# Kernel optimization log

Measured on AMD Instinct MI355X. Metric: run time of the kernel, lower is better.

## Reference

```python
import jax, jax.numpy as jnp
import numpy as np

B, S, D = 2, 2048, 2048
NH, NKV, HD = 16, 4, 128
REP = NH // NKV
EPS = 1e-6
ROPE_THETA = 1e6


def setup_inputs() -> dict:
    key = jax.random.key(0)
    ks = jax.random.split(key, 6)
    x = jax.random.normal(ks[0], (B, S, D), jnp.float32)
    # real rotary embeddings: [S, HD]
    inv_freq = 1.0 / (ROPE_THETA ** (np.arange(0, HD, 2, dtype=np.float64) / HD))
    freqs = np.outer(np.arange(S, dtype=np.float64), inv_freq)
    emb = np.concatenate([freqs, freqs], axis=-1)
    cos = jnp.asarray(np.cos(emb), jnp.float32)
    sin = jnp.asarray(np.sin(emb), jnp.float32)
    scale = 1.0 / np.sqrt(D)
    Wq = jax.random.normal(ks[1], (D, NH * HD), jnp.float32) * scale   # [in, out]
    Wk = jax.random.normal(ks[2], (D, NKV * HD), jnp.float32) * scale
    Wv = jax.random.normal(ks[3], (D, NKV * HD), jnp.float32) * scale
    Wo = jax.random.normal(ks[4], (NH * HD, D), jnp.float32) * (1.0 / np.sqrt(NH * HD))
    q_norm_w = jnp.ones((HD,), jnp.float32)
    k_norm_w = jnp.ones((HD,), jnp.float32)
    return dict(x=x, cos=cos, sin=sin, Wq=Wq, Wk=Wk, Wv=Wv, Wo=Wo,
                q_norm_w=q_norm_w, k_norm_w=k_norm_w)


def _rms_norm(h, w):
    var = jnp.mean(h * h, axis=-1, keepdims=True)
    return w * (h * jax.lax.rsqrt(var + EPS))


def _rotate_half(h):
    h1, h2 = jnp.split(h, 2, axis=-1)
    return jnp.concatenate([-h2, h1], axis=-1)


def reference(x, cos, sin, Wq, Wk, Wv, Wo, q_norm_w, k_norm_w):
    b, s, _ = x.shape
    q = (x @ Wq).reshape(b, s, NH, HD)
    k = (x @ Wk).reshape(b, s, NKV, HD)
    v = (x @ Wv).reshape(b, s, NKV, HD)
    # per-head QK RMSNorm
    q = _rms_norm(q, q_norm_w)
    k = _rms_norm(k, k_norm_w)
    # RoPE: cos/sin [S,HD] -> broadcast over batch and heads
    c = cos[None, :, None, :]
    s_ = sin[None, :, None, :]
    q = q * c + _rotate_half(q) * s_
    k = k * c + _rotate_half(k) * s_
    # GQA: group q heads per kv head instead of materializing repeat_kv
    qg = q.reshape(b, s, NKV, REP, HD)
    scores = jnp.einsum('bqgrd,bkgd->bgrqk', qg, k) / np.sqrt(HD)
    causal = jnp.tril(jnp.ones((s, s), bool))  # [q,k]
    scores = jnp.where(causal, scores, -jnp.inf)
    probs = jax.nn.softmax(scores.astype(jnp.float32), axis=-1).astype(q.dtype)
    out = jnp.einsum('bgrqk,bkgd->bqgrd', probs, v).reshape(b, s, NH * HD)
    return out @ Wo
```

## Files before the change

### kernel.cpp

```cpp
#include <hip/hip_runtime.h>
#include <hip/hip_bf16.h>
#include <math.h>

#define B_ 2
#define S_ 2048
#define D_ 2048
#define NH_ 16
#define NKV_ 4
#define HD_ 128
#define EPS_ 1e-6f
#define SCALE_ 0.08838834764831845f
#define LOG2E_ 1.4426950408889634f
#define KOFF_ 2048
#define VOFF_ 2560

typedef float f32x4 __attribute__((ext_vector_type(4)));
typedef short bf16x8 __attribute__((ext_vector_type(8)));
typedef short short4v __attribute__((ext_vector_type(4)));
typedef float float4v __attribute__((ext_vector_type(4)));
typedef unsigned uint2v __attribute__((ext_vector_type(2)));

static __device__ __forceinline__ short f2bf(float f) {
    union { float f; unsigned u; } x{f};
    unsigned r = (x.u + 0x7fff + ((x.u >> 16) & 1)) >> 16;
    return (short)r;
}
static __device__ __forceinline__ float bf2f(short s) {
    union { unsigned u; float f; } x; x.u = ((unsigned)(unsigned short)s) << 16; return x.f;
}
static __device__ __forceinline__ unsigned pack_bf2(float a, float b) {
    return __builtin_amdgcn_perm(__builtin_bit_cast(unsigned, b),
                                 __builtin_bit_cast(unsigned, a), 0x07060302u);
}

#define AS1(p) ((const __attribute__((address_space(1))) void*)(p))
#define AS3(p) ((__attribute__((address_space(3))) void*)(p))
static __device__ __forceinline__ void async16(const void* g, void* l) {
    __builtin_amdgcn_global_load_lds(AS1(g), AS3(l), 16, 0, 0);
}

__global__ __launch_bounds__(256) void cast_kernel(const float* __restrict__ in,
                                                   short* __restrict__ out) {
    size_t i = ((size_t)blockIdx.x * 256 + threadIdx.x) * 4;
    float4v v = *(const float4v*)(in + i);
    short4v o; o.x = f2bf(v.x); o.y = f2bf(v.y); o.z = f2bf(v.z); o.w = f2bf(v.w);
    *(short4v*)(out + i) = o;
}

__global__ __launch_bounds__(256) void transpose_all_kernel(const float* __restrict__ Wq,
                                                            const float* __restrict__ Wk,
                                                            const float* __restrict__ Wv,
                                                            const float* __restrict__ Wo,
                                                            short* __restrict__ Wt,
                                                            short* __restrict__ Wot) {
    __shared__ float tile[64][65];
    const int bx = blockIdx.x, by = blockIdx.y;
    const float* src; short* dst; int N, nb;
    if (bx < 32)      { src = Wq; dst = Wt;                         N = 2048; nb = bx; }
    else if (bx < 40) { src = Wk; dst = Wt + (size_t)KOFF_ * 2048;  N = 512;  nb = bx - 32; }
    else if (bx < 48) { src = Wv; dst = Wt + (size_t)VOFF_ * 2048;  N = 512;  nb = bx - 40; }
    else              { src = Wo; dst = Wot;                        N = 2048; nb = bx - 48; }
    const int n0 = nb * 64, k0 = by * 64;
    const int tid = threadIdx.x;
    for (int r = 0; r < 16; ++r) {
        int k = r * 4 + (tid >> 6);
        int n = tid & 63;
        tile[k][n] = src[(size_t)(k0 + k) * N + n0 + n];
    }
    __syncthreads();
    for (int r = 0; r < 4; ++r) {
        int n  = r * 16 + (tid >> 4);
        int kk = (tid & 15) * 4;
        short4v o4;
        o4.x = f2bf(tile[kk + 0][n]); o4.y = f2bf(tile[kk + 1][n]);
        o4.z = f2bf(tile[kk + 2][n]); o4.w = f2bf(tile[kk + 3][n]);
        *(short4v*)&dst[(size_t)(n0 + n) * 2048 + k0 + kk] = o4;
    }
}

template<typename TC>
__global__ __launch_bounds__(256) void gemm_tt_kernel(const short* __restrict__ A,
                                                      const short* __restrict__ Bt,
                                                      TC* __restrict__ C,
                                                      int M, int N, int K) {
    __shared__ short As[128 * 32];
    __shared__ short Bs[128 * 32];

    const int tid  = threadIdx.x;
    const int bn   = blockIdx.x, bm = blockIdx.y;
    const int wave = tid >> 6, lane = tid & 63;
    const int quad = lane >> 4, l16 = lane & 15;
    const int wr = wave >> 1, wc = wave & 1;

    f32x4 acc[4][4];
    for (int i = 0; i < 4; ++i)
        for (int j = 0; j < 4; ++j) acc[i][j] = (f32x4){0.f, 0.f, 0.f, 0.f};

    const short* Abase = A  + (size_t)(bm * 128) * K;
    const short* Bbase = Bt + (size_t)(bn * 128) * K;

    int ci0 = wave * 128 + lane;
    for (int k0 = 0; k0 < K; k0 += 32) {
        __syncthreads();
        for (int t = 0; t < 2; ++t) {
            int ci = ci0 + t * 64;
            int r  = ci >> 2;
            int c  = ((ci & 3) - (r >> 1)) & 3;
            size_t goff = (size_t)r * K + k0 + c * 8;
            async16(Abase + goff, &As[ci * 8]);
            async16(Bbase + goff, &Bs[ci * 8]);
        }
        __syncthreads();

        bf16x8 af[4], bfv[4];
        for (int mt = 0; mt < 4; ++mt) {
            int r = wr * 64 + mt * 16 + l16;
            af[mt] = *(const bf16x8*)&As[r * 32 + (((quad + (r >> 1)) & 3) * 8)];
        }
        for (int nt = 0; nt < 4; ++nt) {
            int r = wc * 64 + nt * 16 + l16;
            bfv[nt] = *(const bf16x8*)&Bs[r * 32 + (((quad + (r >> 1)) & 3) * 8)];
        }
        for (int mt = 0; mt < 4; ++mt)
            for (int nt = 0; nt < 4; ++nt)
                acc[mt][nt] = __builtin_amdgcn_mfma_f32_16x16x32_bf16(
                    af[mt], bfv[nt], acc[mt][nt], 0, 0, 0);
    }

    for (int mt = 0; mt < 4; ++mt)
        for (int nt = 0; nt < 4; ++nt)
            for (int j = 0; j < 4; ++j) {
                int row = bm * 128 + wr * 64 + mt * 16 + quad * 4 + j;
                int col = bn * 128 + wc * 64 + nt * 16 + l16;
                float v = acc[mt][nt][j];
                if constexpr (__is_same(TC, short))
                    C[(size_t)row * N + col] = f2bf(v);
                else
                    C[(size_t)row * N + col] = v;
            }
}

__global__ __launch_bounds__(256) void qkv_fused_kernel(const short* __restrict__ xb,
                                                        const short* __restrict__ Wt,
                                                        const float* __restrict__ cosb,
                                                        const float* __restrict__ sinb,
                                                        const float* __restrict__ qw,
                                                        const float* __restrict__ kw,
                                                        short* __restrict__ q_rope,
                                                        short* __restrict__ k_rope,
                                                        short* __restrict__ vtr) {
    __shared__ short tile[128 * 128];
    __shared__ float ss2[2][128];
    short* As = tile;
    short* Bs = tile + 4096;

    const int tid  = threadIdx.x;
    const int bn   = blockIdx.x, bm = blockIdx.y;
    const int wave = tid >> 6, lane = tid & 63;
    const int quad = lane >> 4, l16 = lane & 15;
    const int wr = wave >> 1, wc = wave & 1;

    f32x4 acc[4][4];
    for (int i = 0; i < 4; ++i)
        for (int j = 0; j < 4; ++j) acc[i][j] = (f32x4){0.f, 0.f, 0.f, 0.f};

    const short* Abase = xb + (size_t)(bm * 128) * 2048;
    const short* Bbase = Wt + (size_t)(bn * 128) * 2048;

    int ci0 = wave * 128 + lane;
    for (int k0 = 0; k0 < 2048; k0 += 32) {
        __syncthreads();
        for (int t = 0; t < 2; ++t) {
            int ci = ci0 + t * 64;
            int r  = ci >> 2;
            int c  = ((ci & 3) - (r >> 1)) & 3;
            size_t goff = (size_t)r * 2048 + k0 + c * 8;
            async16(Abase + goff, &As[ci * 8]);
            async16(Bbase + goff, &Bs[ci * 8]);
        }
        __syncthreads();

        bf16x8 af[4], bfv[4];
        for (int mt = 0; mt < 4; ++mt) {
            int r = wr * 64 + mt * 16 + l16;
            af[mt] = *(const bf16x8*)&As[r * 32 + (((quad + (r >> 1)) & 3) * 8)];
        }
        for (int nt = 0; nt < 4; ++nt) {
            int r = wc * 64 + nt * 16 + l16;
            bfv[nt] = *(const bf16x8*)&Bs[r * 32 + (((quad + (r >> 1)) & 3) * 8)];
        }
        for (int mt = 0; mt < 4; ++mt)
            for (int nt = 0; nt < 4; ++nt)
                acc[mt][nt] = __builtin_amdgcn_mfma_f32_16x16x32_bf16(
                    af[mt], bfv[nt], acc[mt][nt], 0, 0, 0);
    }

    if (bn >= 20) {
        const int g = bn - 20;
        for (int mt = 0; mt < 4; ++mt) {
            int tok0 = bm * 128 + wr * 64 + mt * 16 + quad * 4;
            int bb = tok0 >> 11, s0 = tok0 & (S_ - 1);
            for (int nt = 0; nt < 4; ++nt) {
                int d = wc * 64 + nt * 16 + l16;
                short4v o4;
                o4.x = f2bf(acc[mt][nt][0]); o4.y = f2bf(acc[mt][nt][1]);
                o4.z = f2bf(acc[mt][nt][2]); o4.w = f2bf(acc[mt][nt][3]);
                *(short4v*)&vtr[((size_t)(bb * NKV_ + g) * HD_ + d) * S_ + s0] = o4;
            }
        }
        return;
    }

    __syncthreads();
    {
        float pss[4][4];
        for (int mt = 0; mt < 4; ++mt)
            for (int j = 0; j < 4; ++j) {
                float s = 0.f;
                for (int nt = 0; nt < 4; ++nt) s += acc[mt][nt][j] * acc[mt][nt][j];
                pss[mt][j] = s;
            }
        for (int off = 1; off < 16; off <<= 1)
            for (int mt = 0; mt < 4; ++mt)
                for (int j = 0; j < 4; ++j)
                    pss[mt][j] += __shfl_xor(pss[mt][j], off);
        if (l16 == 0)
            for (int mt = 0; mt < 4; ++mt)
                for (int j = 0; j < 4; ++j)
                    ss2[wc][wr * 64 + mt * 16 + quad * 4 + j] = pss[mt][j];
    }
    for (int mt = 0; mt < 4; ++mt)
        for (int nt = 0; nt < 4; ++nt)
            for (int j = 0; j < 4; ++j)
                tile[(wr * 64 + mt * 16 + quad * 4 + j) * 128 + wc * 64 + nt * 16 + l16]
                    = f2bf(acc[mt][nt][j]);
    __syncthreads();

    const bool isQ = (bn < 16);
    const float osc = isQ ? (SCALE_ * LOG2E_) : 1.0f;
    const float* w = isQ ? qw : kw;
    for (int it = 0; it < 8; ++it) {
        int idx = tid + it * 256;
        int row = idx >> 4, seg = idx & 15;
        int tok = bm * 128 + row;
        int bb = tok >> 11, s = tok & (S_ - 1);
        float rstd = rsqrtf((ss2[0][row] + ss2[1][row]) * (1.0f / HD_) + EPS_);
        int c0 = seg * 8, p0 = (seg ^ 8) * 8;
        bf16x8 ta = *(const bf16x8*)&tile[row * 128 + c0];
        bf16x8 tb = *(const bf16x8*)&tile[row * 128 + p0];
        float sgn = (seg < 8) ? -1.0f : 1.0f;
        unsigned ov[4];
        for (int i2 = 0; i2 < 4; ++i2) {
            float r0, r1;
            for (int k = 0; k < 2; ++k) {
                int i = i2 * 2 + k;
                float n1 = bf2f(ta[i]) * rstd * w[c0 + i];
                float n2 = bf2f(tb[i]) * rstd * w[p0 + i];
                float cs = cosb[(size_t)s * HD_ + c0 + i];
                float sn = sinb[(size_t)s * HD_ + c0 + i];
                float o = (n1 * cs + sgn * n2 * sn) * osc;
                if (k == 0) r0 = o; else r1 = o;
            }
            ov[i2] = ((unsigned)(unsigned short)f2bf(r0)) |
                     ((unsigned)(unsigned short)f2bf(r1) << 16);
        }
        short* dst = isQ
            ? q_rope + ((size_t)(bb * S_ + s) * NH_ + bn) * HD_ + c0
            : k_rope + ((size_t)(bb * NKV_ + (bn - 16)) * S_ + s) * HD_ + c0;
        uint2v w0; w0.x = ov[0]; w0.y = ov[1];
        uint2v w1; w1.x = ov[2]; w1.y = ov[3];
        *(uint2v*)dst = w0;
        *(uint2v*)(dst + 4) = w1;
    }
}

__global__ __launch_bounds__(256, 2) void attn_kernel(const short* __restrict__ qr,
                                                      const short* __restrict__ kg,
                                                      const short* __restrict__ vt,
                                                      short* __restrict__ aout) {
    __shared__ short Ks[2][64 * 128];
    __shared__ short Vs[2][128 * 64];

    const int lin = blockIdx.x;
    const int b  = lin & 1;
    const int g  = (lin >> 1) & 3;
    const int hq = (lin >> 3) & 3;
    const int pr = lin >> 5;
    const int h  = g * 4 + hq;

    const int wave = threadIdx.x >> 6, lane = threadIdx.x & 63;
    const int quad = lane >> 4, l16 = lane & 15;

    const short* kbase = kg + (size_t)(b * NKV_ + g) * S_ * HD_;
    const short* vbase = vt + (size_t)(b * NKV_ + g) * HD_ * S_;

    for (int pass = 0; pass < 2; ++pass) {
        const int qt    = pass ? (31 - pr) : pr;
        const int iters = qt + 1;
        const int qrow  = qt * 64 + wave * 16 + l16;

        bf16x8 qf[4];
        {
            const short* qp = qr + ((size_t)(b * S_ + qrow) * NH_ + h) * HD_;
            for (int ks = 0; ks < 4; ++ks)
                qf[ks] = *(const bf16x8*)(qp + ks * 32 + quad * 8);
        }

        f32x4 o[8];
        for (int i = 0; i < 8; ++i) o[i] = (f32x4){0.f, 0.f, 0.f, 0.f};
        float m_i = -INFINITY, l_i = 0.f;

        auto stage = [&](int kt, int bsel) {
            const short* kt_base = kbase + (size_t)kt * 64 * HD_;
            const short* vt_base = vbase + kt * 64;
            for (int t = 0; t < 4; ++t) {
                int ci  = (wave * 4 + t) * 64 + lane;
                int key = ci >> 4;
                int c   = (ci & 15) ^ ((key ^ (key >> 2)) & 15);
                async16(kt_base + key * HD_ + c * 8, &Ks[bsel][ci * 8]);
            }
            for (int t = 0; t < 4; ++t) {
                int ci = (wave * 4 + t) * 64 + lane;
                int d  = ci >> 3;
                int c  = (ci & 7) ^ (d & 7);
                async16(vt_base + (size_t)d * S_ + c * 8, &Vs[bsel][ci * 8]);
            }
        };

        stage(0, 0);
        int buf = 0;
        for (int kt = 0; kt < iters; ++kt) {
            __syncthreads();
            if (kt + 1 < iters) stage(kt + 1, buf ^ 1);

            f32x4 acc[4];
            for (int t = 0; t < 4; ++t) acc[t] = (f32x4){0.f, 0.f, 0.f, 0.f};
            for (int t = 0; t < 4; ++t) {
                int lk = ((t >> 1) << 5) + ((l16 >> 2) << 3) + ((t & 1) << 2) + (l16 & 3);
                const short* kp = &Ks[buf][lk * 128];
                int pm = (lk ^ (lk >> 2)) & 15;
                for (int ks = 0; ks < 4; ++ks) {
                    bf16x8 kf = *(const bf16x8*)(kp + (((ks * 4 + quad) ^ pm) * 8));
                    acc[t] = __builtin_amdgcn_mfma_f32_16x16x32_bf16(kf, qf[ks], acc[t], 0, 0, 0);
                }
            }
            const int key_base = kt * 64;
            if (key_base + 63 > qt * 64 + wave * 16) {
                for (int t = 0; t < 4; ++t)
                    for (int j = 0; j < 4; ++j) {
                        int kl = key_base + ((t >> 1) << 5) + (quad << 3) + ((t & 1) << 2) + j;
                        if (kl > qrow) acc[t][j] = -INFINITY;
                    }
            }
            float mx = m_i;
            for (int t = 0; t < 4; ++t)
                for (int j = 0; j < 4; ++j) mx = fmaxf(mx, acc[t][j]);
            mx = fmaxf(mx, __shfl_xor(mx, 16));
            mx = fmaxf(mx, __shfl_xor(mx, 32));
            float al = __builtin_amdgcn_exp2f(m_i - mx);
            m_i = mx;
            float rs = 0.f;
            float p[4][4];
            for (int t = 0; t < 4; ++t)
                for (int j = 0; j < 4; ++j) {
                    float e = __builtin_amdgcn_exp2f(acc[t][j] - mx);
                    p[t][j] = e;
                    rs += e;
                }
            rs += __shfl_xor(rs, 16);
            rs += __shfl_xor(rs, 32);
            l_i = al * l_i + rs;
            for (int d8 = 0; d8 < 8; ++d8)
                for (int j = 0; j < 4; ++j) o[d8][j] *= al;
            unsigned pk[2][4];
            for (int grp = 0; grp < 2; ++grp) {
                pk[grp][0] = pack_bf2(p[2 * grp][0],     p[2 * grp][1]);
                pk[grp][1] = pack_bf2(p[2 * grp][2],     p[2 * grp][3]);
                pk[grp][2] = pack_bf2(p[2 * grp + 1][0], p[2 * grp + 1][1]);
                pk[grp][3] = pack_bf2(p[2 * grp + 1][2], p[2 * grp + 1][3]);
            }
            for (int grp = 0; grp < 2; ++grp) {
                union { unsigned u[4]; bf16x8 v; } pb;
                for (int i = 0; i < 4; ++i) pb.u[i] = pk[grp][i];
                for (int d8 = 0; d8 < 8; ++d8) {
                    int d = d8 * 16 + l16;
                    bf16x8 vf = *(const bf16x8*)&Vs[buf][d * 64 + (((grp * 4 + quad) ^ (d & 7)) * 8)];
                    o[d8] = __builtin_amdgcn_mfma_f32_16x16x32_bf16(vf, pb.v, o[d8], 0, 0, 0);
                }
            }
            buf ^= 1;
        }
        float il = 1.0f / l_i;
        short* op = aout + ((size_t)(b * S_ + qrow) * NH_ + h) * HD_ + quad * 4;
        for (int d8 = 0; d8 < 8; ++d8) {
            uint2v wv;
            wv.x = ((unsigned)(unsigned short)f2bf(o[d8][0] * il)) |
                   ((unsigned)(unsigned short)f2bf(o[d8][1] * il) << 16);
            wv.y = ((unsigned)(unsigned short)f2bf(o[d8][2] * il)) |
                   ((unsigned)(unsigned short)f2bf(o[d8][3] * il) << 16);
            *(uint2v*)(op + d8 * 16) = wv;
        }
        __syncthreads();
    }
}

extern "C" void kernel_launch(void* const* d_in, const int* in_sizes, int n_in,
                              void* d_out, int out_size, void* d_ws, size_t ws_size,
                              hipStream_t stream) {
    (void)in_sizes; (void)n_in; (void)out_size; (void)ws_size;
    const float* x    = (const float*)d_in[0];
    const float* cosb = (const float*)d_in[1];
    const float* sinb = (const float*)d_in[2];
    const float* Wq   = (const float*)d_in[3];
    const float* Wk   = (const float*)d_in[4];
    const float* Wv   = (const float*)d_in[5];
    const float* Wo   = (const float*)d_in[6];
    const float* qw   = (const float*)d_in[7];
    const float* kw   = (const float*)d_in[8];
    float* out = (float*)d_out;

    char* ws = (char*)d_ws;
    short* xb     = (short*)ws;  ws += (size_t)4096 * 2048 * 2;
    short* Wt     = (short*)ws;  ws += (size_t)3072 * 2048 * 2;
    short* Wot    = (short*)ws;  ws += (size_t)2048 * 2048 * 2;
    short* q_rope = (short*)ws;  ws += (size_t)4096 * 2048 * 2;
    short* k_rope = (short*)ws;  ws += (size_t)4096 * 512 * 2;
    short* vt     = (short*)ws;  ws += (size_t)4096 * 512 * 2;
    short* a_out  = (short*)ws;  ws += (size_t)4096 * 2048 * 2;

    const int M = B_ * S_;

    cast_kernel<<<M * 2048 / 1024, 256, 0, stream>>>(x, xb);
    transpose_all_kernel<<<dim3(80, 32), 256, 0, stream>>>(Wq, Wk, Wv, Wo, Wt, Wot);

    qkv_fused_kernel<<<dim3(24, M / 128), 256, 0, stream>>>(
        xb, Wt, cosb, sinb, qw, kw, q_rope, k_rope, vt);

    attn_kernel<<<512, 256, 0, stream>>>(q_rope, k_rope, vt, a_out);

    gemm_tt_kernel<float><<<dim3(D_ / 128, M / 128), 256, 0, stream>>>(
        a_out, Wot, out, M, D_, 2048);
}
```

Measured before the change: 325.9 us.

## Rewrite QKV GEMM as 256x256 tile, 8-wave, double-buffered async pipeline

The fused QKV projection kernel moves from 128x128 tiles with 4 waves and a synchronous per-k-step load to 256x256 tiles with 8 waves. Async global-to-LDS loads are double-buffered with explicit vmcnt waits and phased barriers, and the LDS layout is XOR-swizzled. The aim is to hide memory latency behind MFMA work and raise data reuse per block. The epilogue now handles two heads per block and uses vectorized cos/sin loads and 16-byte stores. The trade-off is 128KB of LDS per block and a grid of only 192 blocks, which may leave CUs underused.

```diff
diff --git a/kernel.cpp b/kernel.cpp
--- a/kernel.cpp
+++ b/kernel.cpp
@@ -19,6 +19,7 @@
 typedef short short4v __attribute__((ext_vector_type(4)));
 typedef float float4v __attribute__((ext_vector_type(4)));
 typedef unsigned uint2v __attribute__((ext_vector_type(2)));
+typedef unsigned uint4v __attribute__((ext_vector_type(4)));
 
 static __device__ __forceinline__ short f2bf(float f) {
     union { float f; unsigned u; } x{f};
@@ -140,138 +141,230 @@
             }
 }
 
-__global__ __launch_bounds__(256) void qkv_fused_kernel(const short* __restrict__ xb,
-                                                        const short* __restrict__ Wt,
-                                                        const float* __restrict__ cosb,
-                                                        const float* __restrict__ sinb,
-                                                        const float* __restrict__ qw,
-                                                        const float* __restrict__ kw,
-                                                        short* __restrict__ q_rope,
-                                                        short* __restrict__ k_rope,
-                                                        short* __restrict__ vtr) {
-    __shared__ short tile[128 * 128];
-    __shared__ float ss2[2][128];
-    short* As = tile;
-    short* Bs = tile + 4096;
+#define QKV_ITERS 16
+
+__global__ __launch_bounds__(512, 2) void qkv_fused_kernel(const short* __restrict__ xb,
+                                                           const short* __restrict__ Wt,
+                                                           const float* __restrict__ cosb,
+                                                           const float* __restrict__ sinb,
+                                                           const float* __restrict__ qw,
+                                                           const float* __restrict__ kw,
+                                                           short* __restrict__ q_rope,
+                                                           short* __restrict__ k_rope,
+                                                           short* __restrict__ vtr) {
+    __shared__ __align__(16) short smem[65536];
+    __shared__ float ss2[4][256];
+
+    short* A0 = smem;
+    short* A1 = smem + 16384;
+    short* B0 = smem + 32768;
+    short* B1 = smem + 49152;
 
     const int tid  = threadIdx.x;
     const int bn   = blockIdx.x, bm = blockIdx.y;
     const int wave = tid >> 6, lane = tid & 63;
     const int quad = lane >> 4, l16 = lane & 15;
-    const int wr = wave >> 1, wc = wave & 1;
-
-    f32x4 acc[4][4];
-    for (int i = 0; i < 4; ++i)
+    const int wr = wave >> 2, wc = wave & 3;
+
+    const short* Ag = xb + (size_t)(bm * 256) * 2048;
+    const short* Bg = Wt + (size_t)(bn * 256) * 2048;
+
+    f32x4 acc[8][4];
+#pragma unroll
+    for (int i = 0; i < 8; ++i)
+#pragma unroll
         for (int j = 0; j < 4; ++j) acc[i][j] = (f32x4){0.f, 0.f, 0.f, 0.f};
 
-    const short* Abase = xb + (size_t)(bm * 128) * 2048;
-    const short* Bbase = Wt + (size_t)(bn * 128) * 2048;
-
-    int ci0 = wave * 128 + lane;
-    for (int k0 = 0; k0 < 2048; k0 += 32) {
-        __syncthreads();
-        for (int t = 0; t < 2; ++t) {
-            int ci = ci0 + t * 64;
-            int r  = ci >> 2;
-            int c  = ((ci & 3) - (r >> 1)) & 3;
-            size_t goff = (size_t)r * 2048 + k0 + c * 8;
-            async16(Abase + goff, &As[ci * 8]);
-            async16(Bbase + goff, &Bs[ci * 8]);
-        }
-        __syncthreads();
-
-        bf16x8 af[4], bfv[4];
-        for (int mt = 0; mt < 4; ++mt) {
-            int r = wr * 64 + mt * 16 + l16;
-            af[mt] = *(const bf16x8*)&As[r * 32 + (((quad + (r >> 1)) & 3) * 8)];
-        }
-        for (int nt = 0; nt < 4; ++nt) {
-            int r = wc * 64 + nt * 16 + l16;
-            bfv[nt] = *(const bf16x8*)&Bs[r * 32 + (((quad + (r >> 1)) & 3) * 8)];
-        }
-        for (int mt = 0; mt < 4; ++mt)
-            for (int nt = 0; nt < 4; ++nt)
-                acc[mt][nt] = __builtin_amdgcn_mfma_f32_16x16x32_bf16(
-                    af[mt], bfv[nt], acc[mt][nt], 0, 0, 0);
-    }
-
-    if (bn >= 20) {
-        const int g = bn - 20;
-        for (int mt = 0; mt < 4; ++mt) {
-            int tok0 = bm * 128 + wr * 64 + mt * 16 + quad * 4;
+    bf16x8 a[4][2], b0[2][2], b1[2][2];
+
+    auto stage_half = [&](const short* gpanel, int t, int h, short* lslot) {
+#pragma unroll
+        for (int u = 0; u < 2; ++u) {
+            int ci = u * 512 + tid;
+            int r  = ci >> 3;
+            int cb = ((ci & 7) * 16) ^ ((r & 7) << 4);
+            async16(gpanel + (size_t)(h * 128 + r) * 2048 + t * 64 + (cb >> 1),
+                    lslot + h * 8192 + ci * 8);
+        }
+    };
+
+#define LDA_(lbuf, qm) \
+    _Pragma("unroll") for (int mt = 0; mt < 4; ++mt) \
+    _Pragma("unroll") for (int ks = 0; ks < 2; ++ks) { \
+        int row_ = wr * 128 + (qm) * 64 + mt * 16 + l16; \
+        int cb_  = (ks * 64 + quad * 16) ^ ((row_ & 7) << 4); \
+        a[mt][ks] = *(const bf16x8*)&(lbuf)[row_ * 64 + (cb_ >> 1)]; \
+    }
+#define LDB_(lbuf, qn, breg) \
+    _Pragma("unroll") for (int ntl = 0; ntl < 2; ++ntl) \
+    _Pragma("unroll") for (int ks = 0; ks < 2; ++ks) { \
+        int row_ = wc * 64 + (qn) * 32 + ntl * 16 + l16; \
+        int cb_  = (ks * 64 + quad * 16) ^ ((row_ & 7) << 4); \
+        breg[ntl][ks] = *(const bf16x8*)&(lbuf)[row_ * 64 + (cb_ >> 1)]; \
+    }
+#define MFMA16_(qm, qn, breg) \
+    _Pragma("unroll") for (int mt = 0; mt < 4; ++mt) \
+    _Pragma("unroll") for (int ntl = 0; ntl < 2; ++ntl) \
+    _Pragma("unroll") for (int ks = 0; ks < 2; ++ks) \
+        acc[(qm) * 4 + mt][(qn) * 2 + ntl] = __builtin_amdgcn_mfma_f32_16x16x32_bf16( \
+            a[mt][ks], breg[ntl][ks], acc[(qm) * 4 + mt][(qn) * 2 + ntl], 0, 0, 0);
+#define PH_BAR() do { __builtin_amdgcn_sched_barrier(0); __builtin_amdgcn_s_barrier(); } while (0)
+#define PH_MFMA(qm, qn, breg) do { \
+        __builtin_amdgcn_s_setprio(1); MFMA16_(qm, qn, breg); __builtin_amdgcn_s_setprio(0); \
+        __builtin_amdgcn_sched_barrier(0); __builtin_amdgcn_s_barrier(); } while (0)
+
+    stage_half(Bg, 0, 0, B0); stage_half(Bg, 0, 1, B0);
+    stage_half(Ag, 0, 0, A0); stage_half(Ag, 0, 1, A0);
+    stage_half(Bg, 1, 0, B1); stage_half(Bg, 1, 1, B1);
+    asm volatile("s_waitcnt vmcnt(4)" ::: "memory");
+    __builtin_amdgcn_s_barrier();
+
+#pragma unroll 1
+    for (int i = 0; i < QKV_ITERS; ++i) {
+        const int tE = 2 * i, tO = 2 * i + 1;
+        const bool more = (i < QKV_ITERS - 1);
+        LDA_(A0, 0); LDB_(B0, 0, b0);
+        stage_half(Ag, tO, 0, A1);
+        PH_BAR(); PH_MFMA(0, 0, b0);
+
+        LDB_(B0, 1, b1);
+        stage_half(Ag, tO, 1, A1);
+        PH_BAR(); PH_MFMA(0, 1, b1);
+
+        LDA_(A0, 1);
+        if (more) stage_half(Bg, tE + 2, 0, B0);
+        PH_BAR(); PH_MFMA(1, 0, b0);
+
+        if (more) {
+            stage_half(Bg, tE + 2, 1, B0);
+            asm volatile("s_waitcnt vmcnt(4)" ::: "memory");
+        } else {
+            asm volatile("s_waitcnt vmcnt(0)" ::: "memory");
+        }
+        PH_BAR(); PH_MFMA(1, 1, b1);
+
+        LDA_(A1, 0); LDB_(B1, 0, b0);
+        if (more) stage_half(Ag, tE + 2, 0, A0);
+        PH_BAR(); PH_MFMA(0, 0, b0);
+
+        LDB_(B1, 1, b1);
+        if (more) stage_half(Ag, tE + 2, 1, A0);
+        PH_BAR(); PH_MFMA(0, 1, b1);
+
+        LDA_(A1, 1);
+        if (more) stage_half(Bg, tO + 2, 0, B1);
+        PH_BAR(); PH_MFMA(1, 0, b0);
+
+        if (more) {
+            stage_half(Bg, tO + 2, 1, B1);
+            asm volatile("s_waitcnt vmcnt(4)" ::: "memory");
+        } else {
+            asm volatile("s_waitcnt vmcnt(0)" ::: "memory");
+        }
+        PH_BAR(); PH_MFMA(1, 1, b1);
+    }
+
+    if (bn >= 10) {
+        const int gbase = (bn - 10) * 2;
+#pragma unroll
+        for (int am = 0; am < 8; ++am) {
+            int tok0 = bm * 256 + wr * 128 + am * 16 + quad * 4;
             int bb = tok0 >> 11, s0 = tok0 & (S_ - 1);
+#pragma unroll
             for (int nt = 0; nt < 4; ++nt) {
-                int d = wc * 64 + nt * 16 + l16;
+                int col = wc * 64 + nt * 16 + l16;
+                int g = gbase + (col >> 7);
+                int d = col & 127;
                 short4v o4;
-                o4.x = f2bf(acc[mt][nt][0]); o4.y = f2bf(acc[mt][nt][1]);
-                o4.z = f2bf(acc[mt][nt][2]); o4.w = f2bf(acc[mt][nt][3]);
+                o4.x = f2bf(acc[am][nt][0]); o4.y = f2bf(acc[am][nt][1]);
+                o4.z = f2bf(acc[am][nt][2]); o4.w = f2bf(acc[am][nt][3]);
                 *(short4v*)&vtr[((size_t)(bb * NKV_ + g) * HD_ + d) * S_ + s0] = o4;
             }
         }
         return;
     }
 
-    __syncthreads();
     {
-        float pss[4][4];
-        for (int mt = 0; mt < 4; ++mt)
+        float pss[8][4];
+#pragma unroll
+        for (int am = 0; am < 8; ++am)
+#pragma unroll
             for (int j = 0; j < 4; ++j) {
                 float s = 0.f;
-                for (int nt = 0; nt < 4; ++nt) s += acc[mt][nt][j] * acc[mt][nt][j];
-                pss[mt][j] = s;
-            }
+#pragma unroll
+                for (int nt = 0; nt < 4; ++nt) s += acc[am][nt][j] * acc[am][nt][j];
+                pss[am][j] = s;
+            }
+#pragma unroll
         for (int off = 1; off < 16; off <<= 1)
-            for (int mt = 0; mt < 4; ++mt)
+#pragma unroll
+            for (int am = 0; am < 8; ++am)
+#pragma unroll
                 for (int j = 0; j < 4; ++j)
-                    pss[mt][j] += __shfl_xor(pss[mt][j], off);
+                    pss[am][j] += __shfl_xor(pss[am][j], off);
         if (l16 == 0)
-            for (int mt = 0; mt < 4; ++mt)
+#pragma unroll
+            for (int am = 0; am < 8; ++am)
+#pragma unroll
                 for (int j = 0; j < 4; ++j)
-                    ss2[wc][wr * 64 + mt * 16 + quad * 4 + j] = pss[mt][j];
-    }
-    for (int mt = 0; mt < 4; ++mt)
+                    ss2[wc][wr * 128 + am * 16 + quad * 4 + j] = pss[am][j];
+    }
+    short* ct = smem;
+#pragma unroll
+    for (int am = 0; am < 8; ++am)
+#pragma unroll
         for (int nt = 0; nt < 4; ++nt)
+#pragma unroll
             for (int j = 0; j < 4; ++j)
-                tile[(wr * 64 + mt * 16 + quad * 4 + j) * 128 + wc * 64 + nt * 16 + l16]
-                    = f2bf(acc[mt][nt][j]);
+                ct[(wr * 128 + am * 16 + quad * 4 + j) * 256 + wc * 64 + nt * 16 + l16]
+                    = f2bf(acc[am][nt][j]);
     __syncthreads();
 
-    const bool isQ = (bn < 16);
+    const bool isQ = (bn < 8);
     const float osc = isQ ? (SCALE_ * LOG2E_) : 1.0f;
     const float* w = isQ ? qw : kw;
-    for (int it = 0; it < 8; ++it) {
-        int idx = tid + it * 256;
-        int row = idx >> 4, seg = idx & 15;
-        int tok = bm * 128 + row;
+#pragma unroll 1
+    for (int it = 0; it < 16; ++it) {
+        int idx = it * 512 + tid;
+        int row = idx >> 5;
+        int s32 = idx & 31;
+        int head = s32 >> 4, seg = s32 & 15;
+        int tok = bm * 256 + row;
         int bb = tok >> 11, s = tok & (S_ - 1);
-        float rstd = rsqrtf((ss2[0][row] + ss2[1][row]) * (1.0f / HD_) + EPS_);
+        float rstd = rsqrtf((ss2[2 * head][row] + ss2[2 * head + 1][row]) * (1.0f / HD_) + EPS_);
         int c0 = seg * 8, p0 = (seg ^ 8) * 8;
-        bf16x8 ta = *(const bf16x8*)&tile[row * 128 + c0];
-        bf16x8 tb = *(const bf16x8*)&tile[row * 128 + p0];
+        bf16x8 ta = *(const bf16x8*)&ct[row * 256 + head * 128 + c0];
+        bf16x8 tb = *(const bf16x8*)&ct[row * 256 + head * 128 + p0];
         float sgn = (seg < 8) ? -1.0f : 1.0f;
-        unsigned ov[4];
-        for (int i2 = 0; i2 < 4; ++i2) {
-            float r0, r1;
-            for (int k = 0; k < 2; ++k) {
-                int i = i2 * 2 + k;
-                float n1 = bf2f(ta[i]) * rstd * w[c0 + i];
-                float n2 = bf2f(tb[i]) * rstd * w[p0 + i];
-                float cs = cosb[(size_t)s * HD_ + c0 + i];
-                float sn = sinb[(size_t)s * HD_ + c0 + i];
-                float o = (n1 * cs + sgn * n2 * sn) * osc;
-                if (k == 0) r0 = o; else r1 = o;
-            }
-            ov[i2] = ((unsigned)(unsigned short)f2bf(r0)) |
-                     ((unsigned)(unsigned short)f2bf(r1) << 16);
-        }
+        float4v cs0 = *(const float4v*)&cosb[(size_t)s * HD_ + c0];
+        float4v cs1 = *(const float4v*)&cosb[(size_t)s * HD_ + c0 + 4];
+        float4v sn0 = *(const float4v*)&sinb[(size_t)s * HD_ + c0];
+        float4v sn1 = *(const float4v*)&sinb[(size_t)s * HD_ + c0 + 4];
+        float ov[8];
+#pragma unroll
+        for (int i = 0; i < 8; ++i) {
+            float n1 = bf2f(ta[i]) * rstd * w[c0 + i];
+            float n2 = bf2f(tb[i]) * rstd * w[p0 + i];
+            float cs = (i < 4) ? cs0[i & 3] : cs1[i & 3];
+            float sn = (i < 4) ? sn0[i & 3] : sn1[i & 3];
+            ov[i] = (n1 * cs + sgn * n2 * sn) * osc;
+        }
+        uint4v wv;
+#pragma unroll
+        for (int i2 = 0; i2 < 4; ++i2)
+            wv[i2] = ((unsigned)(unsigned short)f2bf(ov[2 * i2])) |
+                     ((unsigned)(unsigned short)f2bf(ov[2 * i2 + 1]) << 16);
+        int gh = isQ ? (bn * 2 + head) : ((bn - 8) * 2 + head);
         short* dst = isQ
-            ? q_rope + ((size_t)(bb * S_ + s) * NH_ + bn) * HD_ + c0
-            : k_rope + ((size_t)(bb * NKV_ + (bn - 16)) * S_ + s) * HD_ + c0;
-        uint2v w0; w0.x = ov[0]; w0.y = ov[1];
-        uint2v w1; w1.x = ov[2]; w1.y = ov[3];
-        *(uint2v*)dst = w0;
-        *(uint2v*)(dst + 4) = w1;
-    }
+            ? q_rope + ((size_t)(bb * S_ + s) * NH_ + gh) * HD_ + c0
+            : k_rope + ((size_t)(bb * NKV_ + gh) * S_ + s) * HD_ + c0;
+        *(uint4v*)dst = wv;
+    }
+#undef LDA_
+#undef LDB_
+#undef MFMA16_
+#undef PH_BAR
+#undef PH_MFMA
 }
 
 __global__ __launch_bounds__(256, 2) void attn_kernel(const short* __restrict__ qr,
@@ -433,7 +526,7 @@
     cast_kernel<<<M * 2048 / 1024, 256, 0, stream>>>(x, xb);
     transpose_all_kernel<<<dim3(80, 32), 256, 0, stream>>>(Wq, Wk, Wv, Wo, Wt, Wot);
 
-    qkv_fused_kernel<<<dim3(24, M / 128), 256, 0, stream>>>(
+    qkv_fused_kernel<<<dim3(12, M / 256), 512, 0, stream>>>(
         xb, Wt, cosb, sinb, qw, kw, q_rope, k_rope, vt);
 
     attn_kernel<<<512, 256, 0, stream>>>(q_rope, k_rope, vt, a_out);
```

Result: faster. 308.4 us (-5.4%).
